# Kernel tuning notes

Hardware: AMD Instinct MI355X
Metric: run time of the kernel (lower is better)

## Reference

```python
import jax, jax.numpy as jnp
import numpy as np

N_NODES = 30000
N_EDGES = 480000
N_GRAPHS = 500
D_IN = 78


def gcn_conv(x, W, b, src, dst, n_nodes):
    """PyG GCNConv: add self-loops, sym-normalize, linear then aggregate, bias after."""
    xw = x @ W  # [N, d_out]
    deg = jnp.zeros((n_nodes,), x.dtype).at[dst].add(1.0) + 1.0  # +1 self-loop
    dinv = jax.lax.rsqrt(deg)
    norm = dinv[src] * dinv[dst]  # [E]
    msg = xw[src] * norm[:, None]  # [E, d_out] edge gather
    out = jnp.zeros_like(xw).at[dst].add(msg)  # scatter-add to dst
    out = out + xw * (dinv * dinv)[:, None]  # self-loop contribution
    return out + b


def setup_inputs() -> dict:
    key = jax.random.key(0)
    ks = jax.random.split(key, 16)
    x = jax.random.normal(ks[0], (N_NODES, D_IN), dtype=jnp.float32)
    edge_index = jax.random.randint(ks[1], (2, N_EDGES), 0, N_NODES, dtype=jnp.int32)
    batch = jnp.sort(jax.random.randint(ks[2], (N_NODES,), 0, N_GRAPHS, dtype=jnp.int32))

    def lin(k, fi, fo):
        s = 1.0 / np.sqrt(fi)
        k1, k2 = jax.random.split(k)
        W = jax.random.uniform(k1, (fi, fo), jnp.float32, -s, s)
        b = jax.random.uniform(k2, (fo,), jnp.float32, -s, s)
        return W, b

    W1, b1 = lin(ks[3], D_IN, D_IN)
    W2, b2 = lin(ks[4], D_IN, D_IN * 2)
    W3, b3 = lin(ks[5], D_IN * 2, D_IN * 4)
    Wf1, bf1 = lin(ks[6], D_IN * 4, 1024)
    Wf2, bf2 = lin(ks[7], 1024, 128)
    return {"x": x, "edge_index": edge_index, "batch": batch,
            "W1": W1, "b1": b1, "W2": W2, "b2": b2, "W3": W3, "b3": b3,
            "Wf1": Wf1, "bf1": bf1, "Wf2": Wf2, "bf2": bf2}


def reference(x, edge_index, batch, W1, b1, W2, b2, W3, b3, Wf1, bf1, Wf2, bf2):
    src, dst = edge_index[0], edge_index[1]
    n = x.shape[0]
    h = jax.nn.relu(gcn_conv(x, W1, b1, src, dst, n))
    h = jax.nn.relu(gcn_conv(h, W2, b2, src, dst, n))
    h = jax.nn.relu(gcn_conv(h, W3, b3, src, dst, n))
    # global max pool over graphs
    pooled = jax.ops.segment_max(h, batch, num_segments=N_GRAPHS)  # [G, 312]
    pooled = jnp.where(jnp.isfinite(pooled), pooled, 0.0)  # guard empty segments
    out = jax.nn.relu(pooled @ Wf1 + bf1)
    out = out @ Wf2 + bf2  # dropout is identity in eval mode
    return out
```

## Files before the change

kernel.cpp:

```cpp
#include <hip/hip_runtime.h>

#define NODES  30000
#define EDGES  480000
#define GRAPHS 500
#define MPAD   30016
#define NB     118

typedef __bf16 bf16x8 __attribute__((ext_vector_type(8)));
typedef float  f32x4  __attribute__((ext_vector_type(4)));

__device__ __forceinline__ float4 f4add(float4 a, float4 b) {
    a.x += b.x; a.y += b.y; a.z += b.z; a.w += b.w; return a;
}
__device__ __forceinline__ float4 f4max(float4 a, float4 b) {
    a.x = fmaxf(a.x, b.x); a.y = fmaxf(a.y, b.y);
    a.z = fmaxf(a.z, b.z); a.w = fmaxf(a.w, b.w); return a;
}

__device__ __forceinline__ void split_f32(float a, unsigned short& hi, unsigned short& lo) {
    unsigned int u = __float_as_uint(a);
    unsigned int rh = (u + 0x7fffu + ((u >> 16) & 1u)) & 0xffff0000u;
    hi = (unsigned short)(rh >> 16);
    float l = a - __uint_as_float(rh);
    unsigned int ul = __float_as_uint(l);
    lo = (unsigned short)((ul + 0x7fffu + ((ul >> 16) & 1u)) >> 16);
}

__device__ __forceinline__ void gload_lds16(const void* g, void* l) {
    __builtin_amdgcn_global_load_lds(
        (__attribute__((address_space(1))) void*)g,
        (__attribute__((address_space(3))) void*)l, 16, 0, 0);
}

__global__ void count_kernel(const int* __restrict__ dst, int* __restrict__ cnt, int E) {
    int i = blockIdx.x * blockDim.x + threadIdx.x;
    if (i < E) atomicAdd(&cnt[dst[i]], 1);
}

__global__ __launch_bounds__(256) void scan_bsum_kernel(const int* __restrict__ cnt,
                                                        int* __restrict__ bsum, int n) {
    __shared__ int buf[256];
    int t = threadIdx.x;
    int i = blockIdx.x * 256 + t;
    buf[t] = (i < n) ? cnt[i] : 0;
    __syncthreads();
    for (int ofs = 128; ofs > 0; ofs >>= 1) {
        if (t < ofs) buf[t] += buf[t + ofs];
        __syncthreads();
    }
    if (t == 0) bsum[blockIdx.x] = buf[0];
}

__global__ __launch_bounds__(128) void scan_top_kernel(const int* __restrict__ bsum,
                                                       int* __restrict__ boff) {
    __shared__ int buf[128];
    int t = threadIdx.x;
    int own = (t < NB) ? bsum[t] : 0;
    buf[t] = own;
    __syncthreads();
    for (int ofs = 1; ofs < 128; ofs <<= 1) {
        int v = (t >= ofs) ? buf[t - ofs] : 0;
        __syncthreads();
        buf[t] += v;
        __syncthreads();
    }
    if (t < NB) boff[t] = buf[t] - own;
}

__global__ __launch_bounds__(256) void scan_apply_kernel(const int* __restrict__ cnt,
                                                         const int* __restrict__ boff,
                                                         int* __restrict__ rowstart,
                                                         float* __restrict__ dinv, int n) {
    __shared__ int buf[256];
    int t = threadIdx.x;
    int i = blockIdx.x * 256 + t;
    int own = (i < n) ? cnt[i] : 0;
    buf[t] = own;
    __syncthreads();
    for (int ofs = 1; ofs < 256; ofs <<= 1) {
        int v = (t >= ofs) ? buf[t - ofs] : 0;
        __syncthreads();
        buf[t] += v;
        __syncthreads();
    }
    if (i < n) {
        rowstart[i] = boff[blockIdx.x] + buf[t] - own;
        dinv[i] = rsqrtf((float)own + 1.0f);
    }
}

__global__ void fill_kernel(const int* __restrict__ src, const int* __restrict__ dst,
                            const int* __restrict__ rowstart, int* __restrict__ cursor,
                            int* __restrict__ csr_src, int E) {
    int i = blockIdx.x * blockDim.x + threadIdx.x;
    if (i < E) {
        int d = dst[i];
        int pos = atomicAdd(&cursor[d], 1);
        csr_src[rowstart[d] + pos] = src[i];
    }
}

__global__ void prescale_kernel(const float* __restrict__ X, const float* __restrict__ dinv,
                                float* __restrict__ Xs, int total) {
    int i = blockIdx.x * blockDim.x + threadIdx.x;
    if (i < total) {
        int node = i / 80;
        int c = i - node * 80;
        Xs[i] = (c < 78) ? X[node * 78 + c] * dinv[node] : 0.0f;
    }
}

__global__ void wsplit_kernel(const float* __restrict__ W, unsigned short* __restrict__ hi,
                              unsigned short* __restrict__ lo, int K, int N, int Kp) {
    int n = blockIdx.x, k = threadIdx.x;
    float v = (n < N && k < K) ? W[(size_t)k * N + n] : 0.0f;
    unsigned short h, l;
    split_f32(v, h, l);
    hi[(size_t)n * Kp + k] = h;
    lo[(size_t)n * Kp + k] = l;
}

template <int DV, int KQ, int SPLIT>
__global__ __launch_bounds__(256) void agg_split_v4(
    const float* __restrict__ Xs, const int* __restrict__ rowstart,
    const int* __restrict__ cnt, const int* __restrict__ csr_src,
    const float* __restrict__ dinv,
    unsigned short* __restrict__ ohi, unsigned short* __restrict__ olo)
{
    constexpr int EPI = 64 / DV;
    constexpr int Kp  = KQ * 4 * SPLIT;
    constexpr int DVS = DV * SPLIT;
    int task = blockIdx.x * 4 + (threadIdx.x >> 6);
    int node = (SPLIT == 1) ? task : (task >> 1);
    int hh   = (SPLIT == 1) ? 0    : (task & (SPLIT - 1));
    int cb   = hh * DV;
    int lane = threadIdx.x & 63;
    int sub = lane / DV;
    int c4 = lane - sub * DV;
    const float4* X4 = (const float4*)Xs;

    float4 acc0 = {0.f, 0.f, 0.f, 0.f}, acc1 = {0.f, 0.f, 0.f, 0.f};
    float4 acc2 = {0.f, 0.f, 0.f, 0.f}, acc3 = {0.f, 0.f, 0.f, 0.f};
    int s = rowstart[node];
    int e = s + cnt[node];

    if (sub < EPI) {
        if (sub == 0) acc0 = X4[(size_t)node * DVS + cb + c4];
        int j = s;
        for (; j + 8 * EPI <= e; j += 8 * EPI) {
            int i0 = csr_src[j + sub],           i1 = csr_src[j + EPI + sub];
            int i2 = csr_src[j + 2 * EPI + sub], i3 = csr_src[j + 3 * EPI + sub];
            int i4 = csr_src[j + 4 * EPI + sub], i5 = csr_src[j + 5 * EPI + sub];
            int i6 = csr_src[j + 6 * EPI + sub], i7 = csr_src[j + 7 * EPI + sub];
            float4 x0 = X4[(size_t)i0 * DVS + cb + c4], x1 = X4[(size_t)i1 * DVS + cb + c4];
            float4 x2 = X4[(size_t)i2 * DVS + cb + c4], x3 = X4[(size_t)i3 * DVS + cb + c4];
            float4 x4 = X4[(size_t)i4 * DVS + cb + c4], x5 = X4[(size_t)i5 * DVS + cb + c4];
            float4 x6 = X4[(size_t)i6 * DVS + cb + c4], x7 = X4[(size_t)i7 * DVS + cb + c4];
            acc0 = f4add(acc0, x0); acc1 = f4add(acc1, x1);
            acc2 = f4add(acc2, x2); acc3 = f4add(acc3, x3);
            acc0 = f4add(acc0, x4); acc1 = f4add(acc1, x5);
            acc2 = f4add(acc2, x6); acc3 = f4add(acc3, x7);
        }
        for (; j + 4 * EPI <= e; j += 4 * EPI) {
            int i0 = csr_src[j + sub],           i1 = csr_src[j + EPI + sub];
            int i2 = csr_src[j + 2 * EPI + sub], i3 = csr_src[j + 3 * EPI + sub];
            float4 x0 = X4[(size_t)i0 * DVS + cb + c4], x1 = X4[(size_t)i1 * DVS + cb + c4];
            float4 x2 = X4[(size_t)i2 * DVS + cb + c4], x3 = X4[(size_t)i3 * DVS + cb + c4];
            acc0 = f4add(acc0, x0); acc1 = f4add(acc1, x1);
            acc2 = f4add(acc2, x2); acc3 = f4add(acc3, x3);
        }
        for (; j < e; j += EPI) {
            int jj = j + sub;
            if (jj < e) {
                int idx = csr_src[jj];
                acc0 = f4add(acc0, X4[(size_t)idx * DVS + cb + c4]);
            }
        }
    }
    float4 acc = f4add(f4add(acc0, acc1), f4add(acc2, acc3));

    if constexpr (EPI > 1) {
        float sx[EPI - 1], sy[EPI - 1], sz[EPI - 1], sw[EPI - 1];
        #pragma unroll
        for (int sft = 1; sft < EPI; sft++) {
            sx[sft - 1] = __shfl(acc.x, lane + sft * DV);
            sy[sft - 1] = __shfl(acc.y, lane + sft * DV);
            sz[sft - 1] = __shfl(acc.z, lane + sft * DV);
            sw[sft - 1] = __shfl(acc.w, lane + sft * DV);
        }
        #pragma unroll
        for (int sft = 1; sft < EPI; sft++) {
            acc.x += sx[sft - 1];
            acc.y += sy[sft - 1];
            acc.z += sz[sft - 1];
            acc.w += sw[sft - 1];
        }
    }

    if (lane < KQ) {
        float di = (lane < DV) ? dinv[node] : 0.0f;
        ushort4 h4, l4;
        split_f32(acc.x * di, h4.x, l4.x);
        split_f32(acc.y * di, h4.y, l4.y);
        split_f32(acc.z * di, h4.z, l4.z);
        split_f32(acc.w * di, h4.w, l4.w);
        size_t off = (size_t)node * Kp + (size_t)(cb + lane) * 4;
        *(ushort4*)&ohi[off] = h4;
        *(ushort4*)&olo[off] = l4;
    }
}

template <int NCK>
__global__ __launch_bounds__(256) void mfma_gemm_v2(
    const unsigned short* __restrict__ Ahi, const unsigned short* __restrict__ Alo,
    const unsigned short* __restrict__ Bhi, const unsigned short* __restrict__ Blo,
    const float* __restrict__ bias, const float* __restrict__ scale,
    float* __restrict__ C, int M, int N, int Cstride, int nN, int do_relu)
{
    constexpr int Kp = NCK * 32;
    constexpr int CELLS = NCK * 256;
    extern __shared__ unsigned short smem[];
    unsigned short* sA = smem;
    unsigned short* sB = smem + 2 * CELLS * 8;

    int t = threadIdx.x;
    int wv = t >> 6, ln = t & 63;
    int q = ln >> 4, l16 = ln & 15;
    int wm = wv & 1, wn = wv >> 1;
    int m0 = blockIdx.x * 64;

    #pragma unroll
    for (int i = 0; i < 2 * NCK; i++) {
        int c = i * 256 + t;
        int plane = c / CELLS;
        int r = c - plane * CELLS;
        int ck = r >> 8, qq = (r >> 6) & 3, row = r & 63;
        const unsigned short* src = (plane ? Alo : Ahi) + (size_t)(m0 + row) * Kp + ck * 32 + qq * 8;
        gload_lds16(src, &sA[(size_t)c * 8]);
    }

    for (int nt = 0; nt < nN; nt++) {
        int n0 = nt * 64;
        if (nt > 0) __syncthreads();
        #pragma unroll
        for (int i = 0; i < 2 * NCK; i++) {
            int c = i * 256 + t;
            int plane = c / CELLS;
            int r = c - plane * CELLS;
            int ck = r >> 8, qq = (r >> 6) & 3, row = r & 63;
            const unsigned short* src = (plane ? Blo : Bhi) + (size_t)(n0 + row) * Kp + ck * 32 + qq * 8;
            gload_lds16(src, &sB[(size_t)c * 8]);
        }
        __syncthreads();

        f32x4 acc[2][2] = {};
        #pragma unroll
        for (int ck = 0; ck < NCK; ck++) {
            bf16x8 ah[2], al[2], bh[2], bl[2];
            #pragma unroll
            for (int i = 0; i < 2; i++) {
                int ra = wm * 32 + i * 16 + l16;
                int rb = wn * 32 + i * 16 + l16;
                ah[i] = *(const bf16x8*)&sA[(size_t)(((0 * NCK + ck) * 4 + q) * 64 + ra) * 8];
                al[i] = *(const bf16x8*)&sA[(size_t)(((1 * NCK + ck) * 4 + q) * 64 + ra) * 8];
                bh[i] = *(const bf16x8*)&sB[(size_t)(((0 * NCK + ck) * 4 + q) * 64 + rb) * 8];
                bl[i] = *(const bf16x8*)&sB[(size_t)(((1 * NCK + ck) * 4 + q) * 64 + rb) * 8];
            }
            #pragma unroll
            for (int i = 0; i < 2; i++)
                #pragma unroll
                for (int j = 0; j < 2; j++) {
                    acc[i][j] = __builtin_amdgcn_mfma_f32_16x16x32_bf16(ah[i], bh[j], acc[i][j], 0, 0, 0);
                    acc[i][j] = __builtin_amdgcn_mfma_f32_16x16x32_bf16(ah[i], bl[j], acc[i][j], 0, 0, 0);
                    acc[i][j] = __builtin_amdgcn_mfma_f32_16x16x32_bf16(al[i], bh[j], acc[i][j], 0, 0, 0);
                }
        }

        #pragma unroll
        for (int i = 0; i < 2; i++) {
            int rbase = m0 + wm * 32 + i * 16 + q * 4;
            #pragma unroll
            for (int j = 0; j < 2; j++) {
                int col = n0 + wn * 32 + j * 16 + l16;
                if (col >= Cstride) continue;
                float bv = (col < N) ? bias[col] : 0.0f;
                #pragma unroll
                for (int r = 0; r < 4; r++) {
                    int row = rbase + r;
                    if (row < M) {
                        float v = 0.0f;
                        if (col < N) {
                            v = acc[i][j][r] + bv;
                            if (do_relu) v = fmaxf(v, 0.0f);
                            if (scale) v *= scale[row];
                        }
                        C[(size_t)row * Cstride + col] = v;
                    }
                }
            }
        }
    }
}

__device__ inline int lower_bound_dev(const int* a, int n, int v) {
    int lo = 0, hi = n;
    while (lo < hi) { int mid = (lo + hi) >> 1; if (a[mid] < v) lo = mid + 1; else hi = mid; }
    return lo;
}

__global__ __launch_bounds__(256) void pool_kernel(const float* __restrict__ H,
                                                   const int* __restrict__ batch,
                                                   float* __restrict__ pooled, int n, int G) {
    __shared__ float4 red[3][78];
    int g = blockIdx.x;
    int t = threadIdx.x;
    int s = lower_bound_dev(batch, n, g);
    int e = lower_bound_dev(batch, n, g + 1);
    int rg = t / 78, c = t - rg * 78;
    const float4* H4 = (const float4*)H;
    if (rg < 3) {
        float4 m = {0.f, 0.f, 0.f, 0.f};
        for (int i = s + rg; i < e; i += 3)
            m = f4max(m, H4[(size_t)i * 78 + c]);
        red[rg][c] = m;
    }
    __syncthreads();
    if (t < 78) {
        float4 m = f4max(f4max(red[0][t], red[1][t]), red[2][t]);
        ((float4*)pooled)[(size_t)g * 78 + t] = m;
    }
}

__global__ __launch_bounds__(256) void fc1_kernel(const float* __restrict__ pooled,
                                                  const float* __restrict__ Wf1,
                                                  const float* __restrict__ bf1,
                                                  float* __restrict__ f1buf) {
    __shared__ float pl[4][312];
    int cb = blockIdx.x, gb = blockIdx.y;
    int t = threadIdx.x;
    for (int i = t; i < 4 * 312; i += 256) {
        int g = i / 312, k = i - g * 312;
        pl[g][k] = pooled[(size_t)(gb * 4 + g) * 312 + k];
    }
    __syncthreads();
    int col = cb * 256 + t;
    float a0 = 0.f, a1 = 0.f, a2 = 0.f, a3 = 0.f;
    #pragma unroll 4
    for (int k = 0; k < 312; k++) {
        float w = Wf1[(size_t)k * 1024 + col];
        a0 += pl[0][k] * w; a1 += pl[1][k] * w; a2 += pl[2][k] * w; a3 += pl[3][k] * w;
    }
    float b = bf1[col];
    int g0 = gb * 4;
    f1buf[(size_t)g0 * 1024 + col]       = fmaxf(a0 + b, 0.f);
    f1buf[(size_t)(g0 + 1) * 1024 + col] = fmaxf(a1 + b, 0.f);
    f1buf[(size_t)(g0 + 2) * 1024 + col] = fmaxf(a2 + b, 0.f);
    f1buf[(size_t)(g0 + 3) * 1024 + col] = fmaxf(a3 + b, 0.f);
}

__global__ __launch_bounds__(256) void fc2_part_kernel(const float* __restrict__ f1buf,
                                                       const float* __restrict__ Wf2,
                                                       float* __restrict__ partial) {
    __shared__ float f1s[4][128];
    __shared__ float red[256][4];
    int kt = blockIdx.x;
    int gb = blockIdx.y;
    int t = threadIdx.x;
    int col = t & 127, ks = t >> 7;
    for (int i = t; i < 512; i += 256) {
        int g = i >> 7, k = i & 127;
        f1s[g][k] = f1buf[(size_t)(gb * 4 + g) * 1024 + kt * 128 + k];
    }
    __syncthreads();
    float a0 = 0.f, a1 = 0.f, a2 = 0.f, a3 = 0.f;
    const float* w2 = Wf2 + (size_t)(kt * 128 + ks * 64) * 128 + col;
    #pragma unroll 4
    for (int k = 0; k < 64; k++) {
        float w = w2[(size_t)k * 128];
        int kk = ks * 64 + k;
        a0 += f1s[0][kk] * w; a1 += f1s[1][kk] * w; a2 += f1s[2][kk] * w; a3 += f1s[3][kk] * w;
    }
    red[t][0] = a0; red[t][1] = a1; red[t][2] = a2; red[t][3] = a3;
    __syncthreads();
    if (t < 128) {
        #pragma unroll
        for (int g = 0; g < 4; g++)
            partial[((size_t)kt * GRAPHS + gb * 4 + g) * 128 + col] = red[t][g] + red[t + 128][g];
    }
}

__global__ void fc2_reduce_kernel(const float* __restrict__ partial, const float* __restrict__ bf2,
                                  float* __restrict__ out, int total) {
    int i = blockIdx.x * blockDim.x + threadIdx.x;
    if (i < total) {
        float s = bf2[i & 127];
        #pragma unroll
        for (int kt = 0; kt < 8; kt++) s += partial[(size_t)kt * total + i];
        out[i] = s;
    }
}

extern "C" void kernel_launch(void* const* d_in, const int* in_sizes, int n_in,
                              void* d_out, int out_size, void* d_ws, size_t ws_size,
                              hipStream_t stream) {
    const float* x    = (const float*)d_in[0];
    const int*   ei   = (const int*)d_in[1];
    const int*   batch= (const int*)d_in[2];
    const float* W1 = (const float*)d_in[3];  const float* b1  = (const float*)d_in[4];
    const float* W2 = (const float*)d_in[5];  const float* b2  = (const float*)d_in[6];
    const float* W3 = (const float*)d_in[7];  const float* b3  = (const float*)d_in[8];
    const float* Wf1= (const float*)d_in[9];  const float* bf1 = (const float*)d_in[10];
    const float* Wf2= (const float*)d_in[11]; const float* bf2 = (const float*)d_in[12];
    float* out = (float*)d_out;

    const int* srcp = ei;
    const int* dstp = ei + EDGES;

    char* p = (char*)d_ws;
    size_t o = 0;
    auto takeB = [&](size_t bytes) { char* q = p + o; o += (bytes + 255) & ~(size_t)255; return q; };
    int*   cnt      = (int*)takeB(NODES * 4);
    int*   cursor   = (int*)takeB(NODES * 4);
    int*   rowstart = (int*)takeB(NODES * 4);
    int*   bsum     = (int*)takeB(NB * 4);
    int*   boff     = (int*)takeB(NB * 4);
    float* dinv     = (float*)takeB(NODES * 4);
    int*   csr_src  = (int*)takeB(EDGES * 4);
    unsigned short* aggH = (unsigned short*)takeB((size_t)MPAD * 160 * 2);
    unsigned short* aggL = (unsigned short*)takeB((size_t)MPAD * 160 * 2);
    float* xs      = (float*)takeB((size_t)NODES * 80 * 4);
    float* hbuf    = (float*)takeB((size_t)NODES * 312 * 4);
    float* pooled  = (float*)takeB((size_t)GRAPHS * 312 * 4);
    float* f1buf   = (float*)takeB((size_t)GRAPHS * 1024 * 4);
    float* partial = (float*)takeB((size_t)8 * GRAPHS * 128 * 4);
    unsigned short* Wt1h = (unsigned short*)takeB(128 * 96 * 2);
    unsigned short* Wt1l = (unsigned short*)takeB(128 * 96 * 2);
    unsigned short* Wt2h = (unsigned short*)takeB(192 * 96 * 2);
    unsigned short* Wt2l = (unsigned short*)takeB(192 * 96 * 2);
    unsigned short* Wt3h = (unsigned short*)takeB(320 * 160 * 2);
    unsigned short* Wt3l = (unsigned short*)takeB(320 * 160 * 2);
    (void)ws_size;

    hipMemsetAsync(cnt, 0, NODES * sizeof(int), stream);
    hipMemsetAsync(cursor, 0, NODES * sizeof(int), stream);

    wsplit_kernel<<<128, 96, 0, stream>>>(W1, Wt1h, Wt1l, 78, 78, 96);
    wsplit_kernel<<<192, 96, 0, stream>>>(W2, Wt2h, Wt2l, 78, 156, 96);
    wsplit_kernel<<<320, 160, 0, stream>>>(W3, Wt3h, Wt3l, 156, 312, 160);

    count_kernel<<<(EDGES + 255) / 256, 256, 0, stream>>>(dstp, cnt, EDGES);
    scan_bsum_kernel<<<NB, 256, 0, stream>>>(cnt, bsum, NODES);
    scan_top_kernel<<<1, 128, 0, stream>>>(bsum, boff);
    scan_apply_kernel<<<NB, 256, 0, stream>>>(cnt, boff, rowstart, dinv, NODES);
    fill_kernel<<<(EDGES + 255) / 256, 256, 0, stream>>>(srcp, dstp, rowstart, cursor, csr_src, EDGES);

    const int NBLK = MPAD / 64;

    prescale_kernel<<<(NODES * 80 + 255) / 256, 256, 0, stream>>>(x, dinv, xs, NODES * 80);
    agg_split_v4<20, 24, 1><<<NODES / 4, 256, 0, stream>>>(xs, rowstart, cnt, csr_src, dinv, aggH, aggL);
    mfma_gemm_v2<3><<<NBLK, 256, 3 * 16384, stream>>>(aggH, aggL, Wt1h, Wt1l, b1, dinv, hbuf,
                                                      NODES, 78, 80, 2, 1);
    agg_split_v4<20, 24, 1><<<NODES / 4, 256, 0, stream>>>(hbuf, rowstart, cnt, csr_src, dinv, aggH, aggL);
    mfma_gemm_v2<3><<<NBLK, 256, 3 * 16384, stream>>>(aggH, aggL, Wt2h, Wt2l, b2, dinv, hbuf,
                                                      NODES, 156, 160, 3, 1);
    agg_split_v4<20, 20, 2><<<NODES * 2 / 4, 256, 0, stream>>>(hbuf, rowstart, cnt, csr_src, dinv, aggH, aggL);
    mfma_gemm_v2<5><<<NBLK, 256, 5 * 16384, stream>>>(aggH, aggL, Wt3h, Wt3l, b3, nullptr, hbuf,
                                                      NODES, 312, 312, 5, 1);

    pool_kernel<<<GRAPHS, 256, 0, stream>>>(hbuf, batch, pooled, NODES, GRAPHS);
    fc1_kernel<<<dim3(4, GRAPHS / 4), 256, 0, stream>>>(pooled, Wf1, bf1, f1buf);
    fc2_part_kernel<<<dim3(8, GRAPHS / 4), 256, 0, stream>>>(f1buf, Wf2, partial);
    fc2_reduce_kernel<<<(GRAPHS * 128 + 255) / 256, 256, 0, stream>>>(partial, bf2, out, GRAPHS * 128);
}
```

Baseline: 363.2 us.

## Merge setup kernels and use one wavefront per node for layer-3 aggregation

Three weight-split launches and the edge count are merged into one prep kernel, and the CSR fill and input prescale become a second merged kernel. The cursor is now zeroed inside scan_apply, which drops a memset. Layer-3 aggregation drops the two-wavefront feature split and uses DV=40 with one wavefront per node, so each edge index is read once. In exchange, EPI becomes 1, giving less edge parallelism per wavefront, and 24 lanes sit idle.

Result: faster. 346.2 us (-4.7%).

```diff
diff --git a/kernel.cpp b/kernel.cpp
--- a/kernel.cpp
+++ b/kernel.cpp
@@ -32,9 +32,30 @@
         (__attribute__((address_space(3))) void*)l, 16, 0, 0);
 }
 
-__global__ void count_kernel(const int* __restrict__ dst, int* __restrict__ cnt, int E) {
-    int i = blockIdx.x * blockDim.x + threadIdx.x;
-    if (i < E) atomicAdd(&cnt[dst[i]], 1);
+__global__ __launch_bounds__(256) void prep_kernel(
+    const float* __restrict__ W1, const float* __restrict__ W2, const float* __restrict__ W3,
+    unsigned short* __restrict__ h1, unsigned short* __restrict__ l1,
+    unsigned short* __restrict__ h2, unsigned short* __restrict__ l2,
+    unsigned short* __restrict__ h3, unsigned short* __restrict__ l3,
+    const int* __restrict__ dst, int* __restrict__ cnt)
+{
+    int b = blockIdx.x, t = threadIdx.x;
+    if (b < 640) {
+        const float* W; unsigned short *oh, *ol; int n, K, N, Kp;
+        if (b < 128)      { W = W1; oh = h1; ol = l1; n = b;       K = 78;  N = 78;  Kp = 96;  }
+        else if (b < 320) { W = W2; oh = h2; ol = l2; n = b - 128; K = 78;  N = 156; Kp = 96;  }
+        else              { W = W3; oh = h3; ol = l3; n = b - 320; K = 156; N = 312; Kp = 160; }
+        if (t < Kp) {
+            float v = (n < N && t < K) ? W[(size_t)t * N + n] : 0.0f;
+            unsigned short h, l;
+            split_f32(v, h, l);
+            oh[(size_t)n * Kp + t] = h;
+            ol[(size_t)n * Kp + t] = l;
+        }
+    } else {
+        int i = (b - 640) * 256 + t;
+        if (i < EDGES) atomicAdd(&cnt[dst[i]], 1);
+    }
 }
 
 __global__ __launch_bounds__(256) void scan_bsum_kernel(const int* __restrict__ cnt,
@@ -70,6 +91,7 @@
 __global__ __launch_bounds__(256) void scan_apply_kernel(const int* __restrict__ cnt,
                                                          const int* __restrict__ boff,
                                                          int* __restrict__ rowstart,
+                                                         int* __restrict__ cursor,
                                                          float* __restrict__ dinv, int n) {
     __shared__ int buf[256];
     int t = threadIdx.x;
@@ -85,42 +107,35 @@
     }
     if (i < n) {
         rowstart[i] = boff[blockIdx.x] + buf[t] - own;
+        cursor[i] = 0;
         dinv[i] = rsqrtf((float)own + 1.0f);
     }
 }
 
-__global__ void fill_kernel(const int* __restrict__ src, const int* __restrict__ dst,
-                            const int* __restrict__ rowstart, int* __restrict__ cursor,
-                            int* __restrict__ csr_src, int E) {
-    int i = blockIdx.x * blockDim.x + threadIdx.x;
-    if (i < E) {
-        int d = dst[i];
-        int pos = atomicAdd(&cursor[d], 1);
-        csr_src[rowstart[d] + pos] = src[i];
-    }
-}
-
-__global__ void prescale_kernel(const float* __restrict__ X, const float* __restrict__ dinv,
-                                float* __restrict__ Xs, int total) {
-    int i = blockIdx.x * blockDim.x + threadIdx.x;
-    if (i < total) {
-        int node = i / 80;
-        int c = i - node * 80;
-        Xs[i] = (c < 78) ? X[node * 78 + c] * dinv[node] : 0.0f;
-    }
-}
-
-__global__ void wsplit_kernel(const float* __restrict__ W, unsigned short* __restrict__ hi,
-                              unsigned short* __restrict__ lo, int K, int N, int Kp) {
-    int n = blockIdx.x, k = threadIdx.x;
-    float v = (n < N && k < K) ? W[(size_t)k * N + n] : 0.0f;
-    unsigned short h, l;
-    split_f32(v, h, l);
-    hi[(size_t)n * Kp + k] = h;
-    lo[(size_t)n * Kp + k] = l;
-}
-
-template <int DV, int KQ, int SPLIT>
+__global__ __launch_bounds__(256) void fill_prescale_kernel(
+    const int* __restrict__ src, const int* __restrict__ dst,
+    const int* __restrict__ rowstart, int* __restrict__ cursor, int* __restrict__ csr_src,
+    const float* __restrict__ X, const float* __restrict__ dinv, float* __restrict__ Xs)
+{
+    int b = blockIdx.x, t = threadIdx.x;
+    if (b < 1875) {
+        int i = b * 256 + t;
+        if (i < EDGES) {
+            int d = dst[i];
+            int pos = atomicAdd(&cursor[d], 1);
+            csr_src[rowstart[d] + pos] = src[i];
+        }
+    } else {
+        int i = (b - 1875) * 256 + t;
+        if (i < NODES * 80) {
+            int node = i / 80;
+            int c = i - node * 80;
+            Xs[i] = (c < 78) ? X[node * 78 + c] * dinv[node] : 0.0f;
+        }
+    }
+}
+
+template <int DV, int KQ>
 __global__ __launch_bounds__(256) void agg_split_v4(
     const float* __restrict__ Xs, const int* __restrict__ rowstart,
     const int* __restrict__ cnt, const int* __restrict__ csr_src,
@@ -128,12 +143,8 @@
     unsigned short* __restrict__ ohi, unsigned short* __restrict__ olo)
 {
     constexpr int EPI = 64 / DV;
-    constexpr int Kp  = KQ * 4 * SPLIT;
-    constexpr int DVS = DV * SPLIT;
-    int task = blockIdx.x * 4 + (threadIdx.x >> 6);
-    int node = (SPLIT == 1) ? task : (task >> 1);
-    int hh   = (SPLIT == 1) ? 0    : (task & (SPLIT - 1));
-    int cb   = hh * DV;
+    constexpr int Kp = KQ * 4;
+    int node = blockIdx.x * 4 + (threadIdx.x >> 6);
     int lane = threadIdx.x & 63;
     int sub = lane / DV;
     int c4 = lane - sub * DV;
@@ -145,17 +156,17 @@
     int e = s + cnt[node];
 
     if (sub < EPI) {
-        if (sub == 0) acc0 = X4[(size_t)node * DVS + cb + c4];
+        if (sub == 0) acc0 = X4[(size_t)node * DV + c4];
         int j = s;
         for (; j + 8 * EPI <= e; j += 8 * EPI) {
             int i0 = csr_src[j + sub],           i1 = csr_src[j + EPI + sub];
             int i2 = csr_src[j + 2 * EPI + sub], i3 = csr_src[j + 3 * EPI + sub];
             int i4 = csr_src[j + 4 * EPI + sub], i5 = csr_src[j + 5 * EPI + sub];
             int i6 = csr_src[j + 6 * EPI + sub], i7 = csr_src[j + 7 * EPI + sub];
-            float4 x0 = X4[(size_t)i0 * DVS + cb + c4], x1 = X4[(size_t)i1 * DVS + cb + c4];
-            float4 x2 = X4[(size_t)i2 * DVS + cb + c4], x3 = X4[(size_t)i3 * DVS + cb + c4];
-            float4 x4 = X4[(size_t)i4 * DVS + cb + c4], x5 = X4[(size_t)i5 * DVS + cb + c4];
-            float4 x6 = X4[(size_t)i6 * DVS + cb + c4], x7 = X4[(size_t)i7 * DVS + cb + c4];
+            float4 x0 = X4[(size_t)i0 * DV + c4], x1 = X4[(size_t)i1 * DV + c4];
+            float4 x2 = X4[(size_t)i2 * DV + c4], x3 = X4[(size_t)i3 * DV + c4];
+            float4 x4 = X4[(size_t)i4 * DV + c4], x5 = X4[(size_t)i5 * DV + c4];
+            float4 x6 = X4[(size_t)i6 * DV + c4], x7 = X4[(size_t)i7 * DV + c4];
             acc0 = f4add(acc0, x0); acc1 = f4add(acc1, x1);
             acc2 = f4add(acc2, x2); acc3 = f4add(acc3, x3);
             acc0 = f4add(acc0, x4); acc1 = f4add(acc1, x5);
@@ -164,8 +175,8 @@
         for (; j + 4 * EPI <= e; j += 4 * EPI) {
             int i0 = csr_src[j + sub],           i1 = csr_src[j + EPI + sub];
             int i2 = csr_src[j + 2 * EPI + sub], i3 = csr_src[j + 3 * EPI + sub];
-            float4 x0 = X4[(size_t)i0 * DVS + cb + c4], x1 = X4[(size_t)i1 * DVS + cb + c4];
-            float4 x2 = X4[(size_t)i2 * DVS + cb + c4], x3 = X4[(size_t)i3 * DVS + cb + c4];
+            float4 x0 = X4[(size_t)i0 * DV + c4], x1 = X4[(size_t)i1 * DV + c4];
+            float4 x2 = X4[(size_t)i2 * DV + c4], x3 = X4[(size_t)i3 * DV + c4];
             acc0 = f4add(acc0, x0); acc1 = f4add(acc1, x1);
             acc2 = f4add(acc2, x2); acc3 = f4add(acc3, x3);
         }
@@ -173,7 +184,7 @@
             int jj = j + sub;
             if (jj < e) {
                 int idx = csr_src[jj];
-                acc0 = f4add(acc0, X4[(size_t)idx * DVS + cb + c4]);
+                acc0 = f4add(acc0, X4[(size_t)idx * DV + c4]);
             }
         }
     }
@@ -204,7 +215,7 @@
         split_f32(acc.y * di, h4.y, l4.y);
         split_f32(acc.z * di, h4.z, l4.z);
         split_f32(acc.w * di, h4.w, l4.w);
-        size_t off = (size_t)node * Kp + (size_t)(cb + lane) * 4;
+        size_t off = (size_t)node * Kp + (size_t)lane * 4;
         *(ushort4*)&ohi[off] = h4;
         *(ushort4*)&olo[off] = l4;
     }
@@ -442,28 +453,25 @@
     (void)ws_size;
 
     hipMemsetAsync(cnt, 0, NODES * sizeof(int), stream);
-    hipMemsetAsync(cursor, 0, NODES * sizeof(int), stream);
-
-    wsplit_kernel<<<128, 96, 0, stream>>>(W1, Wt1h, Wt1l, 78, 78, 96);
-    wsplit_kernel<<<192, 96, 0, stream>>>(W2, Wt2h, Wt2l, 78, 156, 96);
-    wsplit_kernel<<<320, 160, 0, stream>>>(W3, Wt3h, Wt3l, 156, 312, 160);
-
-    count_kernel<<<(EDGES + 255) / 256, 256, 0, stream>>>(dstp, cnt, EDGES);
+
+    prep_kernel<<<640 + 1875, 256, 0, stream>>>(W1, W2, W3, Wt1h, Wt1l, Wt2h, Wt2l,
+                                                Wt3h, Wt3l, dstp, cnt);
     scan_bsum_kernel<<<NB, 256, 0, stream>>>(cnt, bsum, NODES);
     scan_top_kernel<<<1, 128, 0, stream>>>(bsum, boff);
-    scan_apply_kernel<<<NB, 256, 0, stream>>>(cnt, boff, rowstart, dinv, NODES);
-    fill_kernel<<<(EDGES + 255) / 256, 256, 0, stream>>>(srcp, dstp, rowstart, cursor, csr_src, EDGES);
+    scan_apply_kernel<<<NB, 256, 0, stream>>>(cnt, boff, rowstart, cursor, dinv, NODES);
+    fill_prescale_kernel<<<1875 + 9375, 256, 0, stream>>>(srcp, dstp, rowstart, cursor,
+                                                          csr_src, x, dinv, xs);
 
     const int NBLK = MPAD / 64;
-
-    prescale_kernel<<<(NODES * 80 + 255) / 256, 256, 0, stream>>>(x, dinv, xs, NODES * 80);
-    agg_split_v4<20, 24, 1><<<NODES / 4, 256, 0, stream>>>(xs, rowstart, cnt, csr_src, dinv, aggH, aggL);
+    const int AGRID = NODES / 4;
+
+    agg_split_v4<20, 24><<<AGRID, 256, 0, stream>>>(xs, rowstart, cnt, csr_src, dinv, aggH, aggL);
     mfma_gemm_v2<3><<<NBLK, 256, 3 * 16384, stream>>>(aggH, aggL, Wt1h, Wt1l, b1, dinv, hbuf,
                                                       NODES, 78, 80, 2, 1);
-    agg_split_v4<20, 24, 1><<<NODES / 4, 256, 0, stream>>>(hbuf, rowstart, cnt, csr_src, dinv, aggH, aggL);
+    agg_split_v4<20, 24><<<AGRID, 256, 0, stream>>>(hbuf, rowstart, cnt, csr_src, dinv, aggH, aggL);
     mfma_gemm_v2<3><<<NBLK, 256, 3 * 16384, stream>>>(aggH, aggL, Wt2h, Wt2l, b2, dinv, hbuf,
                                                       NODES, 156, 160, 3, 1);
-    agg_split_v4<20, 20, 2><<<NODES * 2 / 4, 256, 0, stream>>>(hbuf, rowstart, cnt, csr_src, dinv, aggH, aggL);
+    agg_split_v4<40, 40><<<AGRID, 256, 0, stream>>>(hbuf, rowstart, cnt, csr_src, dinv, aggH, aggL);
     mfma_gemm_v2<5><<<NBLK, 256, 5 * 16384, stream>>>(aggH, aggL, Wt3h, Wt3l, b3, nullptr, hbuf,
                                                       NODES, 312, 312, 5, 1);
 
```
